# Kernel tuning notes

Hardware: AMD Instinct MI355X
Metric: run time of the kernel (lower is better)

Reference implementation:

```python
import jax, jax.numpy as jnp
import numpy as np

NEG_SLOPE = 0.1  # LeakyReLU negative slope from QuantizationLayer default
C_BINS = 9       # init dim
HID = 100        # mlp_layers hidden width


def leaky_relu(x):
    return jnp.where(x >= 0, x, NEG_SLOPE * x)


def value_layer(ts, w1, b1, w2, b2, w3, b3):
    # ts: [N] scalar inputs -> tiny 3-layer MLP 1->100->100->1 -> [N]
    h = leaky_relu(ts[:, None] * w1[0] + b1)   # [N, HID]
    h = leaky_relu(h @ w2 + b2)                # [N, HID]
    return (h @ w3 + b3)[:, 0]                 # [N]


def setup_inputs() -> dict:
    key = jax.random.key(0)
    ks = jax.random.split(key, 12)
    N, H, W, B = 2_000_000, 256, 336, 8
    x = jax.random.randint(ks[0], (N,), 0, W).astype(jnp.float32)
    y = jax.random.randint(ks[1], (N,), 0, H).astype(jnp.float32)
    t = jax.random.uniform(ks[2], (N,), dtype=jnp.float32)            # normalized timestamp in [0,1]
    p = (jax.random.randint(ks[3], (N,), 0, 2) * 2 - 1).astype(jnp.float32)  # polarity in {-1,+1}
    b = jax.random.randint(ks[4], (N,), 0, B).astype(jnp.float32)
    events = jnp.stack([x, y, t, p, b], axis=1)  # [N,5]
    w1 = jax.random.normal(ks[5], (1, HID), jnp.float32) * 0.5
    b1 = jax.random.normal(ks[6], (HID,), jnp.float32) * 0.1
    w2 = jax.random.normal(ks[7], (HID, HID), jnp.float32) * 0.1
    b2 = jax.random.normal(ks[8], (HID,), jnp.float32) * 0.1
    w3 = jax.random.normal(ks[9], (HID, 1), jnp.float32) * 0.1
    b3 = jax.random.normal(ks[10], (1,), jnp.float32) * 0.1
    return {"events": events, "H": H, "W": W, "B": B,
            "w1": w1, "b1": b1, "w2": w2, "b2": b2, "w3": w3, "b3": b3}


def reference(events, H, W, B, w1, b1, w2, b2, w3, b3):
    C = C_BINS
    x, y, t, p, b = (events[:, i] for i in range(5))
    p01 = (p + 1.0) * 0.5  # {-1,+1} -> {0,1}
    # index into flat voxel buffer of size B*2*C*H*W (no_grad in torch -> stop_gradient)
    idx0 = jax.lax.stop_gradient(
        x.astype(jnp.int32)
        + W * y.astype(jnp.int32)
        + (W * H * C) * p01.astype(jnp.int32)
        + (W * H * C * 2) * b.astype(jnp.int32)
    )
    num_voxels = 2 * C * H * W * B
    vox = jnp.zeros((num_voxels,), dtype=events.dtype)
    for i_bin in range(C):  # static loop over C bins, mirroring the torch loop
        values = t * value_layer(t - i_bin / (C - 1), w1, b1, w2, b2, w3, b3)
        vox = vox.at[idx0 + (W * H) * i_bin].add(values)
    vox = vox.reshape(B, 2, C, H, W)
    return jnp.concatenate([vox[:, 0], vox[:, 1]], axis=1)  # [B, 2C, H, W]
```

## Files before the change

kernel.cpp:

```cpp
#include <hip/hip_runtime.h>


#define HID 100

constexpr int Wd = 336;
constexpr int Hd = 256;
constexpr int Cd = 9;
constexpr int HW = Wd * Hd;
constexpr int PLANE = HW * Cd;
constexpr int BATCH = PLANE * 2;

constexpr int NBUCKET = 4096;
constexpr int CAP = 1024;
constexpr int PB_THREADS = 512;
constexpr int PB_PER_THREAD = 16;
constexpr int PB_EVENTS = PB_THREADS * PB_PER_THREAD;
constexpr int TABLE_N = 2048;

__global__ void zero_kernel(unsigned* __restrict__ p, int n) {
    int i = blockIdx.x * blockDim.x + threadIdx.x;
    if (i < n) p[i] = 0u;
}

__global__ __launch_bounds__(128) void
build_table_kernel(const float* __restrict__ w1,
                   const float* __restrict__ b1,
                   const float* __restrict__ w2,
                   const float* __restrict__ b2,
                   const float* __restrict__ w3,
                   const float* __restrict__ b3,
                   float* __restrict__ table, int table_n) {
    __shared__ float h1[HID];
    __shared__ float partial[128];
    int i = blockIdx.x;
    if (i > table_n) return;
    int tid = threadIdx.x;
    float s = -1.0f + 2.0f * (float)i / (float)table_n;

    if (tid < HID) {
        float h = fmaf(s, w1[tid], b1[tid]);
        h1[tid] = fmaxf(h, 0.1f * h);
    }
    __syncthreads();

    float o = 0.0f;
    if (tid < HID) {
        float a0 = b2[tid], a1 = 0.0f, a2 = 0.0f, a3 = 0.0f;
#pragma unroll
        for (int j = 0; j < HID; j += 4) {
            a0 = fmaf(h1[j + 0], w2[(j + 0) * HID + tid], a0);
            a1 = fmaf(h1[j + 1], w2[(j + 1) * HID + tid], a1);
            a2 = fmaf(h1[j + 2], w2[(j + 2) * HID + tid], a2);
            a3 = fmaf(h1[j + 3], w2[(j + 3) * HID + tid], a3);
        }
        float acc = (a0 + a1) + (a2 + a3);
        float h2 = fmaxf(acc, 0.1f * acc);
        o = h2 * w3[tid];
    }
    partial[tid] = o;
    __syncthreads();
#pragma unroll
    for (int s2 = 64; s2 > 0; s2 >>= 1) {
        if (tid < s2) partial[tid] += partial[tid + s2];
        __syncthreads();
    }
    if (tid == 0) table[i] = partial[0] + b3[0];
}

__global__ __launch_bounds__(PB_THREADS) void
place3_kernel(const float* __restrict__ ev, int n,
              unsigned* __restrict__ gCursor,
              unsigned* __restrict__ bucketData) {
    __shared__ unsigned cnt[NBUCKET];
    __shared__ unsigned base[NBUCKET];
    int tid = threadIdx.x;
    for (int c = tid; c < NBUCKET; c += PB_THREADS) cnt[c] = 0u;
    __syncthreads();

    int ev0 = blockIdx.x * PB_EVENTS;
    unsigned pk[PB_PER_THREAD];
    unsigned meta[PB_PER_THREAD];

#pragma unroll
    for (int j = 0; j < PB_PER_THREAD; ++j) {
        int i = ev0 + tid + j * PB_THREADS;
        if (i < n) {
            const float* e = ev + (size_t)i * 5;
            int p01 = e[3] > 0.0f ? 1 : 0;
            unsigned bucket = (unsigned)(((p01 + 2 * (int)e[4]) << 8) | (int)e[1]);
            unsigned tq = (unsigned)(e[2] * 8388608.0f);
            pk[j] = ((unsigned)(int)e[0] << 23) | tq;
            unsigned r = atomicAdd(&cnt[bucket], 1u);
            meta[j] = (bucket << 13) | r;
        } else {
            meta[j] = 0xFFFFFFFFu;
        }
    }
    __syncthreads();

    for (int c = tid; c < NBUCKET; c += PB_THREADS) {
        unsigned k = cnt[c];
        base[c] = k ? atomicAdd(&gCursor[c], k) : 0u;
    }
    __syncthreads();

#pragma unroll
    for (int j = 0; j < PB_PER_THREAD; ++j) {
        unsigned m = meta[j];
        if (m != 0xFFFFFFFFu) {
            unsigned bucket = m >> 13;
            unsigned pos = base[bucket] + (m & 0x1FFFu);
            if (pos < CAP)
                bucketData[(size_t)bucket * CAP + pos] = pk[j];
        }
    }
}

__global__ __launch_bounds__(256) void
gather7_kernel(const unsigned* __restrict__ gCursor,
               const unsigned* __restrict__ bucketData,
               const float* __restrict__ gtable,
               float* __restrict__ out) {
    __shared__ float table[TABLE_N + 1];
    __shared__ int   head[Wd];
    __shared__ int   nxt[CAP];
    __shared__ unsigned evs[CAP];
    int tid = threadIdx.x;
    int bucket = blockIdx.x;
    for (int i = tid; i < TABLE_N + 1; i += 256) table[i] = gtable[i];
    for (int i = tid; i < Wd; i += 256) head[i] = -1;
    __syncthreads();

    unsigned c = gCursor[bucket];
    if (c > CAP) c = CAP;
    const unsigned* __restrict__ data = bucketData + (size_t)bucket * CAP;

    for (unsigned e = tid; e < c; e += 256) {
        unsigned pkd = data[e];
        evs[e] = pkd;
        int x = (int)(pkd >> 23);
        nxt[e] = atomicExch(&head[x], (int)e);
    }
    __syncthreads();

    int y = bucket & 255;
    int bp = bucket >> 8;
    int b = bp >> 1, p01 = bp & 1;
    size_t rowbase = (size_t)(b * (2 * Cd) + p01 * Cd) * (size_t)HW
                   + (size_t)y * (size_t)Wd;

    for (int x = tid; x < Wd; x += 256) {
        float acc[Cd];
#pragma unroll
        for (int k = 0; k < Cd; ++k) acc[k] = 0.0f;
        for (int e = head[x]; e != -1; e = nxt[e]) {
            unsigned pkd = evs[e];
            float t = (float)(pkd & 0x7FFFFFu) * (1.0f / 8388608.0f);
            float u0 = (t + 1.0f) * (0.5f * (float)TABLE_N);
            int ii0 = (int)u0;
            float fr = u0 - (float)ii0;
#pragma unroll
            for (int k = 0; k < Cd; ++k) {
                int ii = ii0 - 128 * k;
                float t0 = table[ii], t1 = table[ii + 1];
                acc[k] = fmaf(t, fmaf(fr, t1 - t0, t0), acc[k]);
            }
        }
#pragma unroll
        for (int k = 0; k < Cd; ++k)
            out[rowbase + (size_t)k * HW + x] = acc[k];
    }
}

__global__ void zero_out_kernel(float* __restrict__ p, int n) {
    int i = blockIdx.x * blockDim.x + threadIdx.x;
    if (i < n) p[i] = 0.0f;
}

__global__ void scatter_kernel(const float* __restrict__ ev, int n,
                               const float* __restrict__ table, int table_n,
                               float* __restrict__ out) {
    int i = blockIdx.x * blockDim.x + threadIdx.x;
    if (i >= n) return;
    const float* e = ev + (size_t)i * 5;
    float t = e[2];
    int idx0 = (int)e[0] + Wd * (int)e[1] + (e[3] > 0.0f ? PLANE : 0) + BATCH * (int)e[4];
    float half_n = 0.5f * (float)table_n;
#pragma unroll
    for (int k = 0; k < Cd; ++k) {
        float u = (t - 0.125f * (float)k + 1.0f) * half_n;
        int ii = (int)u;
        ii = ii < 0 ? 0 : (ii > table_n - 1 ? table_n - 1 : ii);
        float fr = u - (float)ii;
        float t0 = table[ii], t1 = table[ii + 1];
        atomicAdd(out + (idx0 + k * HW), t * fmaf(fr, t1 - t0, t0));
    }
}

extern "C" void kernel_launch(void* const* d_in, const int* in_sizes, int n_in,
                              void* d_out, int out_size, void* d_ws, size_t ws_size,
                              hipStream_t stream) {
    const float* ev = (const float*)d_in[0];
    const float* w1 = (const float*)d_in[4];
    const float* b1 = (const float*)d_in[5];
    const float* w2 = (const float*)d_in[6];
    const float* b2 = (const float*)d_in[7];
    const float* w3 = (const float*)d_in[8];
    const float* b3 = (const float*)d_in[9];
    float* out = (float*)d_out;
    int n = in_sizes[0] / 5;

    size_t off_table  = 0;
    size_t off_cursor = 8448;
    size_t off_bdata  = off_cursor + (size_t)NBUCKET * 4;
    size_t need       = off_bdata + (size_t)NBUCKET * CAP * 4;

    char* ws = (char*)d_ws;
    float* table = (float*)(ws + off_table);

    if (ws_size >= need) {
        unsigned* gCursor    = (unsigned*)(ws + off_cursor);
        unsigned* bucketData = (unsigned*)(ws + off_bdata);

        hipLaunchKernelGGL(zero_kernel, dim3((NBUCKET + 255) / 256), dim3(256),
                           0, stream, gCursor, NBUCKET);
        hipLaunchKernelGGL(build_table_kernel, dim3(TABLE_N + 1), dim3(128),
                           0, stream, w1, b1, w2, b2, w3, b3, table, TABLE_N);
        hipLaunchKernelGGL(place3_kernel, dim3((n + PB_EVENTS - 1) / PB_EVENTS),
                           dim3(PB_THREADS), 0, stream, ev, n, gCursor, bucketData);
        hipLaunchKernelGGL(gather7_kernel, dim3(NBUCKET), dim3(256), 0, stream,
                           gCursor, bucketData, table, out);
    } else {
        int tn = TABLE_N;
        while (tn > 64 && (size_t)(tn + 1) * sizeof(float) > ws_size) tn >>= 1;
        hipLaunchKernelGGL(zero_out_kernel, dim3((out_size + 255) / 256), dim3(256),
                           0, stream, out, out_size);
        hipLaunchKernelGGL(build_table_kernel, dim3(tn + 1), dim3(128),
                           0, stream, w1, b1, w2, b2, w3, b3, table, tn);
        hipLaunchKernelGGL(scatter_kernel, dim3((n + 255) / 256), dim3(256), 0,
                           stream, ev, n, table, tn, out);
    }
}
```

Measured before the change: 156.1 us.

## Vectorize event loads, stagger cursor atomics, widen gather blocks to cover a row

The placement kernel now loads four consecutive events per thread as five float4 reads instead of scalar strided loads, and rotates the bucket order of the global cursor atomics per block to reduce contention. The gather kernel uses 384 threads so each thread owns one x column without a loop, and copies the lookup table with float4 loads. Event-to-thread assignment changes, so the in-bucket ordering of events changes, and the thread's events become contiguous rather than strided, which may affect load coalescing.

```diff
diff --git a/kernel.cpp b/kernel.cpp
--- a/kernel.cpp
+++ b/kernel.cpp
@@ -16,6 +16,7 @@
 constexpr int PB_PER_THREAD = 16;
 constexpr int PB_EVENTS = PB_THREADS * PB_PER_THREAD;
 constexpr int TABLE_N = 2048;
+constexpr int GT_THREADS = 384;
 
 __global__ void zero_kernel(unsigned* __restrict__ p, int n) {
     int i = blockIdx.x * blockDim.x + threadIdx.x;
@@ -82,23 +83,50 @@
     unsigned meta[PB_PER_THREAD];
 
 #pragma unroll
-    for (int j = 0; j < PB_PER_THREAD; ++j) {
-        int i = ev0 + tid + j * PB_THREADS;
-        if (i < n) {
-            const float* e = ev + (size_t)i * 5;
-            int p01 = e[3] > 0.0f ? 1 : 0;
-            unsigned bucket = (unsigned)(((p01 + 2 * (int)e[4]) << 8) | (int)e[1]);
-            unsigned tq = (unsigned)(e[2] * 8388608.0f);
-            pk[j] = ((unsigned)(int)e[0] << 23) | tq;
-            unsigned r = atomicAdd(&cnt[bucket], 1u);
-            meta[j] = (bucket << 13) | r;
+    for (int j = 0; j < PB_PER_THREAD / 4; ++j) {
+        int i0 = ev0 + (j * PB_THREADS + tid) * 4;
+        float fx[4], fy[4], ft[4], fp[4], fb[4];
+        bool ok4 = (i0 + 3 < n);
+        if (ok4) {
+            const float4* q = (const float4*)(ev + (size_t)i0 * 5);
+            float4 v0 = q[0], v1 = q[1], v2 = q[2], v3 = q[3], v4 = q[4];
+            fx[0]=v0.x; fy[0]=v0.y; ft[0]=v0.z; fp[0]=v0.w; fb[0]=v1.x;
+            fx[1]=v1.y; fy[1]=v1.z; ft[1]=v1.w; fp[1]=v2.x; fb[1]=v2.y;
+            fx[2]=v2.z; fy[2]=v2.w; ft[2]=v3.x; fp[2]=v3.y; fb[2]=v3.z;
+            fx[3]=v3.w; fy[3]=v4.x; ft[3]=v4.y; fp[3]=v4.z; fb[3]=v4.w;
         } else {
-            meta[j] = 0xFFFFFFFFu;
-        }
-    }
-    __syncthreads();
-
-    for (int c = tid; c < NBUCKET; c += PB_THREADS) {
+#pragma unroll
+            for (int k = 0; k < 4; ++k) {
+                int i = i0 + k;
+                if (i < n) {
+                    const float* e = ev + (size_t)i * 5;
+                    fx[k]=e[0]; fy[k]=e[1]; ft[k]=e[2]; fp[k]=e[3]; fb[k]=e[4];
+                } else {
+                    fp[k] = 2.0e9f;
+                }
+            }
+        }
+#pragma unroll
+        for (int k = 0; k < 4; ++k) {
+            int slot = j * 4 + k;
+            int i = i0 + k;
+            if (i < n) {
+                int p01 = fp[k] > 0.0f ? 1 : 0;
+                unsigned bucket = (unsigned)(((p01 + 2 * (int)fb[k]) << 8) | (int)fy[k]);
+                unsigned tq = (unsigned)(ft[k] * 8388608.0f);
+                pk[slot] = ((unsigned)(int)fx[k] << 23) | tq;
+                unsigned r = atomicAdd(&cnt[bucket], 1u);
+                meta[slot] = (bucket << 13) | r;
+            } else {
+                meta[slot] = 0xFFFFFFFFu;
+            }
+        }
+    }
+    __syncthreads();
+
+    unsigned off = ((unsigned)blockIdx.x * 67u) & (NBUCKET - 1);
+    for (int c0 = tid; c0 < NBUCKET; c0 += PB_THREADS) {
+        int c = (int)(((unsigned)c0 + off) & (NBUCKET - 1));
         unsigned k = cnt[c];
         base[c] = k ? atomicAdd(&gCursor[c], k) : 0u;
     }
@@ -116,26 +144,29 @@
     }
 }
 
-__global__ __launch_bounds__(256) void
+__global__ __launch_bounds__(GT_THREADS) void
 gather7_kernel(const unsigned* __restrict__ gCursor,
                const unsigned* __restrict__ bucketData,
                const float* __restrict__ gtable,
                float* __restrict__ out) {
-    __shared__ float table[TABLE_N + 1];
+    __shared__ __align__(16) float table[TABLE_N + 4];
     __shared__ int   head[Wd];
     __shared__ int   nxt[CAP];
     __shared__ unsigned evs[CAP];
     int tid = threadIdx.x;
     int bucket = blockIdx.x;
-    for (int i = tid; i < TABLE_N + 1; i += 256) table[i] = gtable[i];
-    for (int i = tid; i < Wd; i += 256) head[i] = -1;
+    const float4* gt4 = (const float4*)gtable;
+    for (int i = tid; i < TABLE_N / 4; i += GT_THREADS)
+        ((float4*)table)[i] = gt4[i];
+    if (tid == 0) table[TABLE_N] = gtable[TABLE_N];
+    for (int i = tid; i < Wd; i += GT_THREADS) head[i] = -1;
     __syncthreads();
 
     unsigned c = gCursor[bucket];
     if (c > CAP) c = CAP;
     const unsigned* __restrict__ data = bucketData + (size_t)bucket * CAP;
 
-    for (unsigned e = tid; e < c; e += 256) {
+    for (unsigned e = tid; e < c; e += GT_THREADS) {
         unsigned pkd = data[e];
         evs[e] = pkd;
         int x = (int)(pkd >> 23);
@@ -149,7 +180,8 @@
     size_t rowbase = (size_t)(b * (2 * Cd) + p01 * Cd) * (size_t)HW
                    + (size_t)y * (size_t)Wd;
 
-    for (int x = tid; x < Wd; x += 256) {
+    int x = tid;
+    if (x < Wd) {
         float acc[Cd];
 #pragma unroll
         for (int k = 0; k < Cd; ++k) acc[k] = 0.0f;
@@ -228,7 +260,7 @@
                            0, stream, w1, b1, w2, b2, w3, b3, table, TABLE_N);
         hipLaunchKernelGGL(place3_kernel, dim3((n + PB_EVENTS - 1) / PB_EVENTS),
                            dim3(PB_THREADS), 0, stream, ev, n, gCursor, bucketData);
-        hipLaunchKernelGGL(gather7_kernel, dim3(NBUCKET), dim3(256), 0, stream,
+        hipLaunchKernelGGL(gather7_kernel, dim3(NBUCKET), dim3(GT_THREADS), 0, stream,
                            gCursor, bucketData, table, out);
     } else {
         int tn = TABLE_N;
```

New measurement: 155.3 us. No clear change (-0.5%).
